# Performance work log

Hardware: AMD Instinct MI355X
Metric: run time of the kernel (lower is better)

Reference implementation:

```python
import jax, jax.numpy as jnp
import numpy as np

B, T, D, H, O = 64, 512, 256, 1024, 1


def setup_inputs() -> dict:
    key = jax.random.key(0)
    ks = jax.random.split(key, 11)
    s_in = 1.0 / np.sqrt(H)
    def u(k, shape):
        return jax.random.uniform(k, shape, jnp.float32, -s_in, s_in)
    return {
        "x": jax.random.normal(ks[0], (B, T, D), jnp.float32),
        "w_ih_0": u(ks[1], (4 * H, D)),
        "w_hh_0": u(ks[2], (4 * H, H)),
        "b_ih_0": u(ks[3], (4 * H,)),
        "b_hh_0": u(ks[4], (4 * H,)),
        "w_ih_1": u(ks[5], (4 * H, H)),
        "w_hh_1": u(ks[6], (4 * H, H)),
        "b_ih_1": u(ks[7], (4 * H,)),
        "b_hh_1": u(ks[8], (4 * H,)),
        "w_lin": u(ks[9], (O, H)),
        "b_lin": u(ks[10], (O,)),
    }


def _lstm_layer(x, w_ih, w_hh, b_ih, b_hh):
    # x: [B, T, Din] -> h_seq: [B, T, H]. PyTorch gate order: i, f, g, o.
    # Precompute input projections for all timesteps (one big GEMM).
    xp = jnp.einsum("btd,gd->tbg", x, w_ih) + b_ih + b_hh  # [T, B, 4H]
    h0 = jnp.zeros((x.shape[0], w_hh.shape[1]), x.dtype)
    c0 = jnp.zeros_like(h0)

    def step(carry, xp_t):
        h, c = carry
        gates = xp_t + h @ w_hh.T  # [B, 4H]
        i, f, g, o = jnp.split(gates, 4, axis=-1)
        i = jax.nn.sigmoid(i)
        f = jax.nn.sigmoid(f)
        g = jnp.tanh(g)
        o = jax.nn.sigmoid(o)
        c = f * c + i * g
        h = o * jnp.tanh(c)
        return (h, c), h

    (_, _), h_seq = jax.lax.scan(step, (h0, c0), xp)  # h_seq: [T, B, H]
    return jnp.transpose(h_seq, (1, 0, 2))  # [B, T, H]


def reference(x, w_ih_0, w_hh_0, b_ih_0, b_hh_0,
              w_ih_1, w_hh_1, b_ih_1, b_hh_1, w_lin, b_lin):
    h1 = _lstm_layer(x, w_ih_0, w_hh_0, b_ih_0, b_hh_0)
    h2 = _lstm_layer(h1, w_ih_1, w_hh_1, b_ih_1, b_hh_1)
    return h2[:, -1, :] @ w_lin.T + b_lin  # [B, O]
```

## Files before the change

### kernel.cpp

```cpp
#include <hip/hip_runtime.h>


#define T_STEPS 512
#define NWG 256
#define LDS_W     131072
#define LDS_GBUF  (64 * 33 * 4)
#define LDS_CBUF  (64 * 9 * 4)
#define LDS_OFFS  (32 * 4)
#define SMEM_BYTES (LDS_W + LDS_GBUF + LDS_CBUF + LDS_OFFS)

typedef int v2i  __attribute__((ext_vector_type(2)));
typedef int v4i  __attribute__((ext_vector_type(4)));
typedef int v16i __attribute__((ext_vector_type(16)));

__device__ __forceinline__ v16i zero16() {
    v16i z;
#pragma unroll
    for (int i = 0; i < 16; ++i) z[i] = 0;
    return z;
}

__device__ __forceinline__ void load_f16_nw(const char* b0p, v4i* o) {
    const char* b1p = b0p + 4096;
    const char* b2p = b0p + 8192;
    const char* b3p = b0p + 12288;
    asm volatile(
        "global_load_dwordx4 %0, %16, off sc0 sc1\n\t"
        "global_load_dwordx4 %1, %16, off offset:16 sc0 sc1\n\t"
        "global_load_dwordx4 %2, %16, off offset:2048 sc0 sc1\n\t"
        "global_load_dwordx4 %3, %16, off offset:2064 sc0 sc1\n\t"
        "global_load_dwordx4 %4, %17, off sc0 sc1\n\t"
        "global_load_dwordx4 %5, %17, off offset:16 sc0 sc1\n\t"
        "global_load_dwordx4 %6, %17, off offset:2048 sc0 sc1\n\t"
        "global_load_dwordx4 %7, %17, off offset:2064 sc0 sc1\n\t"
        "global_load_dwordx4 %8, %18, off sc0 sc1\n\t"
        "global_load_dwordx4 %9, %18, off offset:16 sc0 sc1\n\t"
        "global_load_dwordx4 %10, %18, off offset:2048 sc0 sc1\n\t"
        "global_load_dwordx4 %11, %18, off offset:2064 sc0 sc1\n\t"
        "global_load_dwordx4 %12, %19, off sc0 sc1\n\t"
        "global_load_dwordx4 %13, %19, off offset:16 sc0 sc1\n\t"
        "global_load_dwordx4 %14, %19, off offset:2048 sc0 sc1\n\t"
        "global_load_dwordx4 %15, %19, off offset:2064 sc0 sc1"
        : "=&v"(o[0]), "=&v"(o[1]), "=&v"(o[2]), "=&v"(o[3]),
          "=&v"(o[4]), "=&v"(o[5]), "=&v"(o[6]), "=&v"(o[7]),
          "=&v"(o[8]), "=&v"(o[9]), "=&v"(o[10]), "=&v"(o[11]),
          "=&v"(o[12]), "=&v"(o[13]), "=&v"(o[14]), "=&v"(o[15])
        : "v"(b0p), "v"(b1p), "v"(b2p), "v"(b3p)
        : "memory");
}

#define WAIT_BIND(cntstr, b)                                                   \
    asm volatile("s_waitcnt vmcnt(" cntstr ")"                                 \
        : "+v"((b)[0]), "+v"((b)[1]), "+v"((b)[2]), "+v"((b)[3]),              \
          "+v"((b)[4]), "+v"((b)[5]), "+v"((b)[6]), "+v"((b)[7]),              \
          "+v"((b)[8]), "+v"((b)[9]), "+v"((b)[10]), "+v"((b)[11]),            \
          "+v"((b)[12]), "+v"((b)[13]), "+v"((b)[14]), "+v"((b)[15])           \
        :: "memory")

__device__ __forceinline__ void st16_wt(void* p, v4i v) {
    asm volatile("global_store_dwordx4 %0, %1, off sc0 sc1" :: "v"(p), "v"(v) : "memory");
}
__device__ __forceinline__ void waitcnt0() {
    asm volatile("s_waitcnt vmcnt(0)" ::: "memory");
}

__device__ __forceinline__ void split_a(v4i A0, v4i A1, v4i& HI, v4i& LO) {
    HI.x = (int)__builtin_amdgcn_perm((unsigned)A0.y, (unsigned)A0.x, 0x07050301u);
    HI.y = (int)__builtin_amdgcn_perm((unsigned)A0.w, (unsigned)A0.z, 0x07050301u);
    HI.z = (int)__builtin_amdgcn_perm((unsigned)A1.y, (unsigned)A1.x, 0x07050301u);
    HI.w = (int)__builtin_amdgcn_perm((unsigned)A1.w, (unsigned)A1.z, 0x07050301u);
    LO.x = (int)(__builtin_amdgcn_perm((unsigned)A0.y, (unsigned)A0.x, 0x06040200u) ^ 0x80808080u);
    LO.y = (int)(__builtin_amdgcn_perm((unsigned)A0.w, (unsigned)A0.z, 0x06040200u) ^ 0x80808080u);
    LO.z = (int)(__builtin_amdgcn_perm((unsigned)A1.y, (unsigned)A1.x, 0x06040200u) ^ 0x80808080u);
    LO.w = (int)(__builtin_amdgcn_perm((unsigned)A1.w, (unsigned)A1.z, 0x06040200u) ^ 0x80808080u);
}

__device__ __forceinline__ void consume8(const v4i* hb, const char* wbase,
                                         v16i& ahh, v16i& amid)
{
#pragma unroll
    for (int s = 0; s < 8; ++s) {
        v4i HI, LO; split_a(hb[2 * s], hb[2 * s + 1], HI, LO);
        v4i BH = *(const v4i*)(wbase + s * 2048);
        v4i BL = *(const v4i*)(wbase + s * 2048 + 1024);
        ahh  = __builtin_amdgcn_mfma_i32_32x32x32_i8(HI, BH, ahh, 0, 0, 0);
        amid = __builtin_amdgcn_mfma_i32_32x32x32_i8(HI, BL, amid, 0, 0, 0);
        amid = __builtin_amdgcn_mfma_i32_32x32x32_i8(LO, BH, amid, 0, 0, 0);
    }
}

__device__ __forceinline__ void kstep(const short* __restrict__ ap,
                                      const char* __restrict__ wl,
                                      v16i& ahh, v16i& amid)
{
    v4i A0 = *(const v4i*)ap;
    v4i A1 = *(const v4i*)(ap + 8);
    v4i HI, LO; split_a(A0, A1, HI, LO);
    v4i BH = *(const v4i*)wl;
    v4i BL = *(const v4i*)(wl + 1024);
    ahh  = __builtin_amdgcn_mfma_i32_32x32x32_i8(HI, BH, ahh, 0, 0, 0);
    amid = __builtin_amdgcn_mfma_i32_32x32x32_i8(HI, BL, amid, 0, 0, 0);
    amid = __builtin_amdgcn_mfma_i32_32x32x32_i8(LO, BH, amid, 0, 0, 0);
}

__global__ void quant_x(const float* __restrict__ x, short* __restrict__ xq, int n)
{
    int i = blockIdx.x * 256 + threadIdx.x;
    if (i < n) {
        float v = x[i] * 2048.f;
        v = fminf(fmaxf(v, -32767.f), 32767.f);
        xq[i] = (short)__float2int_rn(v);
    }
}

__global__ void quant_w(const float* __restrict__ wih0, const float* __restrict__ whh0,
                        const float* __restrict__ wih1, const float* __restrict__ whh1,
                        char* __restrict__ wimg)
{
    int gid = blockIdx.x * 256 + threadIdx.x;
    if (gid >= 256 * 64 * 64) return;
    int lane = gid & 63;
    int s    = (gid >> 6) & 63;
    int wg   = gid >> 12;
    int layer = wg >> 7, nblk = wg & 127;
    int col = nblk * 32 + (lane & 31);
    int ro  = (col & 3) * 1024 + (col >> 2);
    int k0  = s * 32 + (lane >> 5) * 16;
    char* dst = wimg + (size_t)wg * LDS_W + s * 2048 + lane * 16;
#pragma unroll
    for (int j = 0; j < 16; ++j) {
        int k = k0 + j;
        float w = 0.f;
        if (layer == 0) {
            if (k < 256)       w = wih0[ro * 256 + k];
            else if (k < 1280) w = whh0[ro * 1024 + (k - 256)];
        } else {
            if (k < 1024)      w = wih1[ro * 1024 + k];
            else               w = whh1[ro * 1024 + (k - 1024)];
        }
        int q  = __float2int_rn(w * 524288.f);
        int hi = (q + 128) >> 8;
        int lo = q - (hi << 8);
        dst[j]        = (char)hi;
        dst[1024 + j] = (char)lo;
    }
}

__global__ void __launch_bounds__(128) lstm_main(
    const short* __restrict__ xq, const char* __restrict__ wimg,
    const float* __restrict__ bih0, const float* __restrict__ bhh0,
    const float* __restrict__ bih1, const float* __restrict__ bhh1,
    short* __restrict__ h0q, short* __restrict__ h2q,
    float* __restrict__ h2f, unsigned* gslots, unsigned* gbcast)
{
    extern __shared__ char smem[];
    char*  wlds = smem;
    float* gbuf = (float*)(smem + LDS_W);
    float* cbuf = (float*)(smem + LDS_W + LDS_GBUF);
    float* offs = (float*)(smem + LDS_W + LDS_GBUF + LDS_CBUF);

    const int wg    = blockIdx.x;
    const int layer = wg >> 7;
    const int nblk  = wg & 127;
    const int tid   = threadIdx.x;
    const int lane  = tid & 63;
    const int RB    = tid >> 6;
    const float inv30 = 9.313225746154785e-10f;
    const float inv33 = 1.1641532182693481e-10f;

    {
        const v4i* src = (const v4i*)(wimg + (size_t)wg * LDS_W);
        v4i* dst = (v4i*)wlds;
        for (int i = tid; i < LDS_W / 16; i += 128) dst[i] = src[i];
    }
    for (int i = tid; i < 64 * 9; i += 128) cbuf[i] = 0.f;
    __syncthreads();

    if (tid < 32) {
        const int c  = tid;
        const int ns = (layer == 0) ? 40 : 64;
        int cs_x = 0, cs_h = 0;
        for (int s = 0; s < ns; ++s) {
            int sum = 0;
#pragma unroll
            for (int half = 0; half < 2; ++half) {
                const signed char* ph = (const signed char*)(wlds + s * 2048 + (half * 32 + c) * 16);
#pragma unroll
                for (int j = 0; j < 16; ++j)
                    sum += 256 * (int)ph[j] + (int)ph[1024 + j];
            }
            if (layer == 0 && s < 8) cs_x += sum; else cs_h += sum;
        }
        const int col = nblk * 32 + c;
        const int ro  = (col & 3) * 1024 + (col >> 2);
        const float bias = (layer == 0) ? (bih0[ro] + bhh0[ro]) : (bih1[ro] + bhh1[ro]);
        float off = 128.f * (float)cs_h * inv33 + bias;
        if (layer == 0) off += 128.f * (float)cs_x * inv30;
        offs[c] = off;
    }
    __syncthreads();

    const int mrow = RB * 32 + (lane & 31);
    const int ksub = (lane >> 5) * 16;
    const int j0   = nblk * 8;
    const int sj   = j0 >> 5;
    const int hbj  = (j0 >> 4) & 1;
    const int inj  = (j0 & 15) * 2;

    for (int p = 0; p <= T_STEPS + 1; ++p) {
        const bool actL0 = (layer == 0) && (p < T_STEPS);
        const bool actL1 = (layer == 1) && (p >= 2);
        const bool active = actL0 || actL1;

        float px[16];
        v16i ahh = zero16(), amid = zero16();

        if (actL0) {
            v16i ax = zero16(), mx = zero16();
            const short* axp = xq + ((size_t)mrow * 512 + p) * 256 + ksub;
#pragma unroll
            for (int s = 0; s < 8; ++s)
                kstep(axp + s * 32, wlds + s * 2048 + lane * 16, ax, mx);
#pragma unroll
            for (int r = 0; r < 16; ++r)
                px[r] = ((float)ax[r] * 65536.f + (float)mx[r] * 256.f) * inv30;
        } else if (actL1) {
            const char* f0 = (const char*)h0q + ((p - 2) & 3) * 131072
                           + RB * 65536 + lane * 32;
            v4i b0[16], b1[16];
            waitcnt0();
            const char* W = wlds + lane * 16;
            load_f16_nw(f0, b0);
            load_f16_nw(f0 + 16384, b1);
            WAIT_BIND("16", b0); consume8(b0, W, ahh, amid);
            load_f16_nw(f0 + 32768, b0);
            WAIT_BIND("16", b1); consume8(b1, W + 8 * 2048, ahh, amid);
            load_f16_nw(f0 + 49152, b1);
            WAIT_BIND("16", b0); consume8(b0, W + 16 * 2048, ahh, amid);
            WAIT_BIND("0", b1);  consume8(b1, W + 24 * 2048, ahh, amid);
        }

        if (p > 0) {
            const unsigned pp = (unsigned)p;
            if (wg == 0) {
                const unsigned* s0 = gslots + (tid * 2) * 16;
                const unsigned* s1 = s0 + 16;
                while (__hip_atomic_load(s0, __ATOMIC_RELAXED, __HIP_MEMORY_SCOPE_AGENT) < pp)
                    __builtin_amdgcn_s_sleep(1);
                while (__hip_atomic_load(s1, __ATOMIC_RELAXED, __HIP_MEMORY_SCOPE_AGENT) < pp)
                    __builtin_amdgcn_s_sleep(1);
                __syncthreads();
                __hip_atomic_store(gbcast + (tid * 2) * 16, pp, __ATOMIC_RELAXED, __HIP_MEMORY_SCOPE_AGENT);
                __hip_atomic_store(gbcast + (tid * 2 + 1) * 16, pp, __ATOMIC_RELAXED, __HIP_MEMORY_SCOPE_AGENT);
            } else {
                if (tid == 0) {
                    while (__hip_atomic_load(gbcast + wg * 16, __ATOMIC_RELAXED, __HIP_MEMORY_SCOPE_AGENT) < pp)
                        __builtin_amdgcn_s_sleep(1);
                }
            }
            __syncthreads();
            asm volatile("" ::: "memory");
        }

        if (active) {
            float gates[16];
            v4i b0[16], b1[16];
            if (layer == 0) {
                if (p > 0) {
                    const char* f0 = (const char*)h0q + ((p - 1) & 3) * 131072
                                   + RB * 65536 + lane * 32;
                    waitcnt0();
                    const char* W = wlds + lane * 16;
                    load_f16_nw(f0, b0);
                    load_f16_nw(f0 + 16384, b1);
                    WAIT_BIND("16", b0); consume8(b0, W + 8 * 2048, ahh, amid);
                    load_f16_nw(f0 + 32768, b0);
                    WAIT_BIND("16", b1); consume8(b1, W + 16 * 2048, ahh, amid);
                    load_f16_nw(f0 + 49152, b1);
                    WAIT_BIND("16", b0); consume8(b0, W + 24 * 2048, ahh, amid);
                    WAIT_BIND("0", b1);  consume8(b1, W + 32 * 2048, ahh, amid);
                }
#pragma unroll
                for (int r = 0; r < 16; ++r)
                    gates[r] = px[r]
                             + ((float)ahh[r] * 65536.f + (float)amid[r] * 256.f) * inv33
                             + offs[lane & 31];
            } else {
                if (p > 2) {
                    const char* f2 = (const char*)h2q + ((p - 3) & 1) * 131072
                                   + RB * 65536 + lane * 32;
                    waitcnt0();
                    const char* W = wlds + lane * 16;
                    load_f16_nw(f2, b0);
                    load_f16_nw(f2 + 16384, b1);
                    WAIT_BIND("16", b0); consume8(b0, W + 32 * 2048, ahh, amid);
                    load_f16_nw(f2 + 32768, b0);
                    WAIT_BIND("16", b1); consume8(b1, W + 40 * 2048, ahh, amid);
                    load_f16_nw(f2 + 49152, b1);
                    WAIT_BIND("16", b0); consume8(b0, W + 48 * 2048, ahh, amid);
                    WAIT_BIND("0", b1);  consume8(b1, W + 56 * 2048, ahh, amid);
                }
#pragma unroll
                for (int r = 0; r < 16; ++r)
                    gates[r] = ((float)ahh[r] * 65536.f + (float)amid[r] * 256.f) * inv33
                             + offs[lane & 31];
            }
            {
                const int rbase = RB * 32 + 4 * (lane >> 5);
                const int c = lane & 31;
#pragma unroll
                for (int r = 0; r < 16; ++r) {
                    int row = rbase + (r & 3) + 8 * (r >> 2);
                    gbuf[row * 33 + c] = gates[r];
                }
            }
        }
        __syncthreads();
        if (active && tid < 64) {
            const int r = tid;
            unsigned hq[8];
            float hf[8];
#pragma unroll
            for (int u = 0; u < 8; ++u) {
                const float gi = gbuf[r * 33 + 4 * u + 0];
                const float gf = gbuf[r * 33 + 4 * u + 1];
                const float gg = gbuf[r * 33 + 4 * u + 2];
                const float go = gbuf[r * 33 + 4 * u + 3];
                const float i_ = 1.f / (1.f + __expf(-gi));
                const float f_ = 1.f / (1.f + __expf(-gf));
                const float g_ = 1.f - 2.f / (__expf(2.f * gg) + 1.f);
                const float o_ = 1.f / (1.f + __expf(-go));
                float c_ = f_ * cbuf[r * 9 + u] + i_ * g_;
                cbuf[r * 9 + u] = c_;
                const float h_ = o_ * (1.f - 2.f / (__expf(2.f * c_) + 1.f));
                hq[u] = (unsigned)(unsigned short)(short)__float2int_rn(h_ * 16384.f);
                hf[u] = h_;
            }
            v4i pk;
            pk.x = (int)(hq[0] | (hq[1] << 16));
            pk.y = (int)(hq[2] | (hq[3] << 16));
            pk.z = (int)(hq[4] | (hq[5] << 16));
            pk.w = (int)(hq[6] | (hq[7] << 16));
            char* hw = (layer == 0)
                     ? (char*)h0q + (p & 3) * 131072
                     : (char*)h2q + ((p - 2) & 1) * 131072;
            hw += (r >> 5) * 65536 + sj * 2048 + ((r & 31) + 32 * hbj) * 32 + inj;
            st16_wt(hw, pk);
            if (layer == 1 && p == T_STEPS + 1) {
#pragma unroll
                for (int u = 0; u < 8; ++u) h2f[r * 1024 + j0 + u] = hf[u];
            }
        }
        if (p < T_STEPS + 1) {
            waitcnt0();
            __syncthreads();
            if (tid == 0)
                __hip_atomic_store(gslots + wg * 16, (unsigned)(p + 1),
                                   __ATOMIC_RELAXED, __HIP_MEMORY_SCOPE_AGENT);
        }
    }
}

__global__ void final_lin(const float* __restrict__ h2f, const float* __restrict__ wlin,
                          const float* __restrict__ blin, float* __restrict__ out)
{
    const int b = blockIdx.x;
    const int l = threadIdx.x;
    float s = 0.f;
    for (int j = l; j < 1024; j += 64) s += h2f[b * 1024 + j] * wlin[j];
#pragma unroll
    for (int off = 32; off; off >>= 1) s += __shfl_down(s, off);
    if (l == 0) out[b] = s + blin[0];
}

extern "C" void kernel_launch(void* const* d_in, const int* in_sizes, int n_in,
                              void* d_out, int out_size, void* d_ws, size_t ws_size,
                              hipStream_t stream)
{
    const float* x    = (const float*)d_in[0];
    const float* wih0 = (const float*)d_in[1];
    const float* whh0 = (const float*)d_in[2];
    const float* bih0 = (const float*)d_in[3];
    const float* bhh0 = (const float*)d_in[4];
    const float* wih1 = (const float*)d_in[5];
    const float* whh1 = (const float*)d_in[6];
    const float* bih1 = (const float*)d_in[7];
    const float* bhh1 = (const float*)d_in[8];
    const float* wlin = (const float*)d_in[9];
    const float* blin = (const float*)d_in[10];

    char* ws = (char*)d_ws;
    unsigned* gslots = (unsigned*)ws;
    unsigned* gbcast = (unsigned*)(ws + 16384);
    short* h0q = (short*)(ws + 65536);
    short* h2q = (short*)(ws + 65536 + 524288);
    float* h2f = (float*)(ws + 65536 + 786432);
    short* xq  = (short*)(ws + 65536 + 1048576);
    char*  wimg = ws + 65536 + 1048576 + 16777216;

    hipMemsetAsync(ws, 0, 65536, stream);

    quant_x<<<32768, 256, 0, stream>>>(x, xq, 64 * 512 * 256);
    quant_w<<<4096, 256, 0, stream>>>(wih0, whh0, wih1, whh1, wimg);

    hipFuncSetAttribute((const void*)lstm_main,
        hipFuncAttributeMaxDynamicSharedMemorySize, SMEM_BYTES);

    lstm_main<<<NWG, 128, SMEM_BYTES, stream>>>(xq, wimg, bih0, bhh0, bih1, bhh1,
                                                h0q, h2q, h2f, gslots, gbcast);
    final_lin<<<64, 64, 0, stream>>>(h2f, wlin, blin, (float*)d_out);
}
```

Baseline: 4.662 ms.

## Replace centralized grid barrier with decentralized per-layer dependency polling

```diff
diff --git a/kernel.cpp b/kernel.cpp
--- a/kernel.cpp
+++ b/kernel.cpp
@@ -60,6 +60,15 @@
 __device__ __forceinline__ void st16_wt(void* p, v4i v) {
     asm volatile("global_store_dwordx4 %0, %1, off sc0 sc1" :: "v"(p), "v"(v) : "memory");
 }
+__device__ __forceinline__ void store_slot(unsigned* p, unsigned v) {
+    asm volatile("global_store_dword %0, %1, off sc0 sc1" :: "v"(p), "v"(v) : "memory");
+}
+__device__ __forceinline__ v4i ld4_mall(const unsigned* p) {
+    v4i r;
+    asm volatile("global_load_dwordx4 %0, %1, off sc0 sc1\n\ts_waitcnt vmcnt(0)"
+                 : "=v"(r) : "v"(p) : "memory");
+    return r;
+}
 __device__ __forceinline__ void waitcnt0() {
     asm volatile("s_waitcnt vmcnt(0)" ::: "memory");
 }
@@ -151,7 +160,7 @@
     const float* __restrict__ bih0, const float* __restrict__ bhh0,
     const float* __restrict__ bih1, const float* __restrict__ bhh1,
     short* __restrict__ h0q, short* __restrict__ h2q,
-    float* __restrict__ h2f, unsigned* gslots, unsigned* gbcast)
+    float* __restrict__ h2f, unsigned* gslots)
 {
     extern __shared__ char smem[];
     char*  wlds = smem;
@@ -225,7 +234,20 @@
             for (int r = 0; r < 16; ++r)
                 px[r] = ((float)ax[r] * 65536.f + (float)mx[r] * 256.f) * inv30;
         } else if (actL1) {
-            const char* f0 = (const char*)h0q + ((p - 2) & 3) * 131072
+            if (tid < 32) {
+                const unsigned thr = (unsigned)(p - 1);
+                const unsigned* sp = gslots + tid * 4;
+                for (;;) {
+                    v4i v = ld4_mall(sp);
+                    bool ok = ((unsigned)v.x >= thr) && ((unsigned)v.y >= thr) &&
+                              ((unsigned)v.z >= thr) && ((unsigned)v.w >= thr);
+                    if (!__ballot(!ok)) break;
+                    __builtin_amdgcn_s_sleep(3);
+                }
+            }
+            __syncthreads();
+            asm volatile("" ::: "memory");
+            const char* f0 = (const char*)h0q + ((p - 2) & 7) * 131072
                            + RB * 65536 + lane * 32;
             v4i b0[16], b1[16];
             waitcnt0();
@@ -241,21 +263,23 @@
         }
 
         if (p > 0) {
-            const unsigned pp = (unsigned)p;
-            if (wg == 0) {
-                const unsigned* s0 = gslots + (tid * 2) * 16;
-                const unsigned* s1 = s0 + 16;
-                while (__hip_atomic_load(s0, __ATOMIC_RELAXED, __HIP_MEMORY_SCOPE_AGENT) < pp)
-                    __builtin_amdgcn_s_sleep(1);
-                while (__hip_atomic_load(s1, __ATOMIC_RELAXED, __HIP_MEMORY_SCOPE_AGENT) < pp)
-                    __builtin_amdgcn_s_sleep(1);
-                __syncthreads();
-                __hip_atomic_store(gbcast + (tid * 2) * 16, pp, __ATOMIC_RELAXED, __HIP_MEMORY_SCOPE_AGENT);
-                __hip_atomic_store(gbcast + (tid * 2 + 1) * 16, pp, __ATOMIC_RELAXED, __HIP_MEMORY_SCOPE_AGENT);
-            } else {
-                if (tid == 0) {
-                    while (__hip_atomic_load(gbcast + wg * 16, __ATOMIC_RELAXED, __HIP_MEMORY_SCOPE_AGENT) < pp)
-                        __builtin_amdgcn_s_sleep(1);
+            if (tid < 64) {
+                unsigned thr;
+                const unsigned* sp;
+                if (layer == 0) {
+                    sp  = gslots + tid * 4;
+                    thr = (tid < 32) ? (unsigned)p
+                                     : (unsigned)(p > 5 ? p - 5 : 0);
+                } else {
+                    sp  = gslots + 128 + (tid & 31) * 4;
+                    thr = (unsigned)p;
+                }
+                for (;;) {
+                    v4i v = ld4_mall(sp);
+                    bool ok = ((unsigned)v.x >= thr) && ((unsigned)v.y >= thr) &&
+                              ((unsigned)v.z >= thr) && ((unsigned)v.w >= thr);
+                    if (!__ballot(!ok)) break;
+                    __builtin_amdgcn_s_sleep(3);
                 }
             }
             __syncthreads();
@@ -267,7 +291,7 @@
             v4i b0[16], b1[16];
             if (layer == 0) {
                 if (p > 0) {
-                    const char* f0 = (const char*)h0q + ((p - 1) & 3) * 131072
+                    const char* f0 = (const char*)h0q + ((p - 1) & 7) * 131072
                                    + RB * 65536 + lane * 32;
                     waitcnt0();
                     const char* W = wlds + lane * 16;
@@ -287,7 +311,7 @@
                              + offs[lane & 31];
             } else {
                 if (p > 2) {
-                    const char* f2 = (const char*)h2q + ((p - 3) & 1) * 131072
+                    const char* f2 = (const char*)h2q + ((p - 3) & 3) * 131072
                                    + RB * 65536 + lane * 32;
                     waitcnt0();
                     const char* W = wlds + lane * 16;
@@ -342,8 +366,8 @@
             pk.z = (int)(hq[4] | (hq[5] << 16));
             pk.w = (int)(hq[6] | (hq[7] << 16));
             char* hw = (layer == 0)
-                     ? (char*)h0q + (p & 3) * 131072
-                     : (char*)h2q + ((p - 2) & 1) * 131072;
+                     ? (char*)h0q + (p & 7) * 131072
+                     : (char*)h2q + ((p - 2) & 3) * 131072;
             hw += (r >> 5) * 65536 + sj * 2048 + ((r & 31) + 32 * hbj) * 32 + inj;
             st16_wt(hw, pk);
             if (layer == 1 && p == T_STEPS + 1) {
@@ -355,8 +379,7 @@
             waitcnt0();
             __syncthreads();
             if (tid == 0)
-                __hip_atomic_store(gslots + wg * 16, (unsigned)(p + 1),
-                                   __ATOMIC_RELAXED, __HIP_MEMORY_SCOPE_AGENT);
+                store_slot(gslots + wg, (unsigned)(p + 1));
         }
     }
 }
@@ -391,12 +414,11 @@
 
     char* ws = (char*)d_ws;
     unsigned* gslots = (unsigned*)ws;
-    unsigned* gbcast = (unsigned*)(ws + 16384);
     short* h0q = (short*)(ws + 65536);
-    short* h2q = (short*)(ws + 65536 + 524288);
-    float* h2f = (float*)(ws + 65536 + 786432);
-    short* xq  = (short*)(ws + 65536 + 1048576);
-    char*  wimg = ws + 65536 + 1048576 + 16777216;
+    short* h2q = (short*)(ws + 65536 + 1048576);
+    float* h2f = (float*)(ws + 65536 + 1572864);
+    short* xq  = (short*)(ws + 65536 + 1835008);
+    char*  wimg = ws + 65536 + 1835008 + 16777216;
 
     hipMemsetAsync(ws, 0, 65536, stream);
 
@@ -407,6 +429,6 @@
         hipFuncAttributeMaxDynamicSharedMemorySize, SMEM_BYTES);
 
     lstm_main<<<NWG, 128, SMEM_BYTES, stream>>>(xq, wimg, bih0, bhh0, bih1, bhh1,
-                                                h0q, h2q, h2f, gslots, gbcast);
+                                                h0q, h2q, h2f, gslots);
     final_lin<<<64, 64, 0, stream>>>(h2f, wlin, blin, (float*)d_out);
 }
```

After: 4.305 ms. -7.6%, faster.
